# Performance work log

Measured on AMD Instinct MI355X. Metric: run time of the kernel, lower is better.

## Reference

```python
import jax, jax.numpy as jnp
import numpy as np

D_MODEL = 2048
NUM_HEADS = 16
HEAD_DIM = D_MODEL // NUM_HEADS  # 128
B, L = 2, 2048


def setup_inputs() -> dict:
    key = jax.random.key(0)
    ks = jax.random.split(key, 7)
    s = 0.02
    return {
        "x": jax.random.normal(ks[0], (B, L, D_MODEL), dtype=jnp.float32),
        "Wq_w": jax.random.normal(ks[1], (D_MODEL, D_MODEL), dtype=jnp.float32) * s,
        "Wq_b": jnp.zeros((D_MODEL,), dtype=jnp.float32),
        "Wk_w": jax.random.normal(ks[2], (HEAD_DIM, D_MODEL), dtype=jnp.float32) * s,
        "Wk_b": jnp.zeros((HEAD_DIM,), dtype=jnp.float32),
        "Wv_w": jax.random.normal(ks[3], (HEAD_DIM, D_MODEL), dtype=jnp.float32) * s,
        "Wv_b": jnp.zeros((HEAD_DIM,), dtype=jnp.float32),
    }


def reference(x, Wq_w, Wq_b, Wk_w, Wk_b, Wv_w, Wv_b):
    b, l, _ = x.shape
    # torch Linear: y = x @ W.T + b
    Q = (x @ Wq_w.T + Wq_b).reshape(b, l, NUM_HEADS, HEAD_DIM)  # [B,L,H,D]
    K = x @ Wk_w.T + Wk_b  # [B,L,D] single shared KV head (MQA)
    V = x @ Wv_w.T + Wv_b  # [B,L,D]
    scale = 1.0 / jnp.sqrt(jnp.float32(HEAD_DIM))
    # scores: [B,H,Lq,Lk]; K's head dim (size 1 in torch) broadcasts -> contract over d only
    scores = jnp.einsum("bqhd,bkd->bhqk", Q, K) * scale
    attn = jax.nn.softmax(scores, axis=-1)
    out = jnp.einsum("bhqk,bkd->bqhd", attn, V)  # [B,L,H,D]
    return out.reshape(b, l, D_MODEL)
```

## Files before the change

### kernel.cpp

```cpp
#include <hip/hip_runtime.h>
#include <hip/hip_bf16.h>


typedef unsigned short u16;
typedef unsigned int u32;
typedef __bf16 bf16x8 __attribute__((ext_vector_type(8)));
typedef float f32x16 __attribute__((ext_vector_type(16)));
typedef u16 u16x4 __attribute__((ext_vector_type(4)));
typedef u32 u32x4 __attribute__((ext_vector_type(4)));

#define MFMA32(a, b, c) __builtin_amdgcn_mfma_f32_32x32x16_bf16((a), (b), (c), 0, 0, 0)

__device__ __forceinline__ u16 f2bf(float f) {
  __hip_bfloat16 h = __float2bfloat16(f);
  return __builtin_bit_cast(u16, h);
}

__device__ __forceinline__ float fexp2(float x) {
#if __has_builtin(__builtin_amdgcn_exp2f)
  return __builtin_amdgcn_exp2f(x);
#else
  return exp2f(x);
#endif
}

__device__ __forceinline__ void cp16(const void* g, void* l) {
  __builtin_amdgcn_global_load_lds(
      (const __attribute__((address_space(1))) u32*)g,
      (__attribute__((address_space(3))) u32*)l, 16, 0, 0);
}

__device__ __forceinline__ f32x16 zero16() {
  f32x16 v;
#pragma unroll
  for (int i = 0; i < 16; ++i) v[i] = 0.f;
  return v;
}

__global__ __launch_bounds__(256) void k_convert(
    const float* __restrict__ x, const float* __restrict__ wq,
    const float* __restrict__ wk, const float* __restrict__ wv,
    u16* __restrict__ xb, u16* __restrict__ wqb,
    u16* __restrict__ wkb, u16* __restrict__ wvb) {
  int idx = blockIdx.x * 256 + threadIdx.x;
  for (int i = idx; i < 3276800; i += 524288) {
    float4 v; u16* dst;
    if (i < 2097152) {
      v = ((const float4*)x)[i]; dst = xb + (size_t)i * 4;
    } else if (i < 3145728) {
      int j = i - 2097152; v = ((const float4*)wq)[j]; dst = wqb + (size_t)j * 4;
    } else if (i < 3211264) {
      int j = i - 3145728; v = ((const float4*)wk)[j]; dst = wkb + (size_t)j * 4;
    } else {
      int j = i - 3211264; v = ((const float4*)wv)[j]; dst = wvb + (size_t)j * 4;
    }
    u16x4 o;
    o[0] = f2bf(v.x); o[1] = f2bf(v.y); o[2] = f2bf(v.z); o[3] = f2bf(v.w);
    *(u16x4*)dst = o;
  }
}

__global__ __launch_bounds__(256) void k_gemm_qkv(
    const u16* __restrict__ xb, const u16* __restrict__ wqb,
    const u16* __restrict__ wkb, const u16* __restrict__ wvb,
    const float* __restrict__ bq, const float* __restrict__ bk, const float* __restrict__ bv,
    u16* __restrict__ qout, u16* __restrict__ kout, u16* __restrict__ vtout) {
  __shared__ __align__(16) u16 sh[10240];
  const int tid = threadIdx.x;
  const int w = tid >> 6, lane = tid & 63, ln = lane & 31, hi = lane >> 5;
  const int wr = w >> 1, wc = w & 1;
  const int m0 = blockIdx.x * 128;
  const int by = blockIdx.y;
  const int mode = (by < 16) ? 0 : (by - 15);
  const int n0loc = (mode == 0) ? by * 128 : 0;
  const u16* __restrict__ Bp = (mode == 0) ? wqb : (mode == 1 ? wkb : wvb);
  const u16* Arow = xb + (size_t)m0 * 2048;
  const u16* Brow = Bp + (size_t)n0loc * 2048;

  const u16* sb[5];
#pragma unroll
  for (int i = 0; i < 5; ++i) {
    int s = (w + i * 4) * 64 + lane;
    const u16* base; int r, c;
    if (s < 640) { r = s / 5; c = s % 5; if (c > 3) c = 0; base = Arow; }
    else { int s2 = s - 640; r = s2 / 5; c = s2 % 5; if (c > 3) c = 0; base = Brow; }
    sb[i] = base + (size_t)r * 2048 + c * 8;
  }

  f32x16 acc[2][2];
  acc[0][0] = zero16(); acc[0][1] = zero16(); acc[1][0] = zero16(); acc[1][1] = zero16();

  const int a0off = (wr * 64 + ln) * 40 + hi * 8;
  const int b0off = 5120 + (wc * 64 + ln) * 40 + hi * 8;

  for (int k0 = 0; k0 < 2048; k0 += 32) {
    __syncthreads();
#pragma unroll
    for (int i = 0; i < 5; ++i)
      cp16(sb[i] + k0, (void*)(sh + (w + i * 4) * 512));
    __syncthreads();
#pragma unroll
    for (int kc = 0; kc < 2; ++kc) {
      const int ko = kc * 16;
      bf16x8 a0 = *(const bf16x8*)&sh[a0off + ko];
      bf16x8 a1 = *(const bf16x8*)&sh[a0off + 1280 + ko];
      bf16x8 b0 = *(const bf16x8*)&sh[b0off + ko];
      bf16x8 b1 = *(const bf16x8*)&sh[b0off + 1280 + ko];
      acc[0][0] = MFMA32(a0, b0, acc[0][0]);
      acc[0][1] = MFMA32(a0, b1, acc[0][1]);
      acc[1][0] = MFMA32(a1, b0, acc[1][0]);
      acc[1][1] = MFMA32(a1, b1, acc[1][1]);
    }
  }

  const float qscale = 0.12751744630098356f;
#pragma unroll
  for (int fm = 0; fm < 2; ++fm) {
#pragma unroll
    for (int fn = 0; fn < 2; ++fn) {
      f32x16 a = acc[fm][fn];
      const int mbase = m0 + wr * 64 + fm * 32;
      const int nloc = n0loc + wc * 64 + fn * 32 + ln;
      if (mode == 0) {
        const float bsc = bq[nloc] * qscale;
#pragma unroll
        for (int r = 0; r < 16; ++r) {
          int row = (r & 3) + 8 * (r >> 2) + 4 * hi;
          qout[(size_t)(mbase + row) * 2048 + nloc] = f2bf(a[r] * qscale + bsc);
        }
      } else if (mode == 1) {
        const float bb = bk[nloc];
#pragma unroll
        for (int r = 0; r < 16; ++r) {
          int row = (r & 3) + 8 * (r >> 2) + 4 * hi;
          kout[(size_t)(mbase + row) * 128 + nloc] = f2bf(a[r] + bb);
        }
      } else {
        const float bb = bv[nloc];
#pragma unroll
        for (int r = 0; r < 16; ++r) {
          int row = (r & 3) + 8 * (r >> 2) + 4 * hi;
          int m = mbase + row;
          vtout[(size_t)((m >> 11) * 128 + nloc) * 2048 + (m & 2047)] = f2bf(a[r] + bb);
        }
      }
    }
  }
}

__global__ __launch_bounds__(256, 1) void k_attn(
    const u16* __restrict__ qb, const u16* __restrict__ kb, const u16* __restrict__ vtb,
    float* __restrict__ out) {
  __shared__ __align__(16) u16 sh[35840];
  const int tid = threadIdx.x;
  const int w = tid >> 6, lane = tid & 63, ln = lane & 31, hi = lane >> 5;
  const int q0 = blockIdx.x * 256, h = blockIdx.y, b = blockIdx.z;
  const size_t bL = (size_t)b * 2048;
  const u16* kbase = kb + bL * 128;
  const u16* vbase = vtb + (size_t)b * 128 * 2048;

  bf16x8 qfA[8], qfB[8];
  {
    const u16* qrowA = qb + (bL + q0 + w * 64 + ln) * 2048 + h * 128 + hi * 8;
    const u16* qrowB = qrowA + 32 * 2048;
#pragma unroll
    for (int kc = 0; kc < 8; ++kc) {
      qfA[kc] = *(const bf16x8*)(qrowA + kc * 16);
      qfB[kc] = *(const bf16x8*)(qrowB + kc * 16);
    }
  }

  const u16* sb[9]; int smul[9];
  const int nsl = (38 - w) >> 2;
#pragma unroll
  for (int i = 0; i < 9; ++i) {
    int sl = w + i * 4;
    if (sl < 35) {
      int s = sl * 64 + lane;
      if (s < 1088) {
        int r = s / 17, c = s % 17; if (c > 15) c = 0;
        sb[i] = kbase + r * 128 + c * 8; smul[i] = 128;
      } else {
        int s2 = s - 1088; int r = s2 / 9, c = s2 % 9; if (c > 7) c = 0;
        sb[i] = vbase + (size_t)r * 2048 + c * 8; smul[i] = 1;
      }
    } else { sb[i] = kbase; smul[i] = 0; }
  }

#pragma unroll
  for (int i = 0; i < 9; ++i)
    if (i < nsl) cp16(sb[i], (void*)(sh + (w + i * 4) * 512));
  __syncthreads();

  f32x16 oA[4], oB[4];
#pragma unroll
  for (int dg = 0; dg < 4; ++dg) { oA[dg] = zero16(); oB[dg] = zero16(); }
  float lA = 0.f, lB = 0.f;

  const int kro = ln * 136 + hi * 8;
  const int vro = 8704 + ln * 72 + hi * 8;

  for (int it = 0; it < 32; ++it) {
    const int cur = (it & 1) * 17920;
    const int nxt = 17920 - cur;
    const size_t k0n = (it < 31) ? (size_t)(it + 1) * 64 : 0;
#pragma unroll
    for (int i = 0; i < 9; ++i)
      if (i < nsl) cp16(sb[i] + k0n * smul[i], (void*)(sh + nxt + (w + i * 4) * 512));

    f32x16 s0A = zero16(), s1A = zero16(), s0B = zero16(), s1B = zero16();
#pragma unroll
    for (int kc = 0; kc < 8; ++kc) {
      bf16x8 a0 = *(const bf16x8*)&sh[cur + kro + kc * 16];
      bf16x8 a1 = *(const bf16x8*)&sh[cur + kro + 32 * 136 + kc * 16];
      s0A = MFMA32(a0, qfA[kc], s0A);
      s1A = MFMA32(a1, qfA[kc], s1A);
      s0B = MFMA32(a0, qfB[kc], s0B);
      s1B = MFMA32(a1, qfB[kc], s1B);
    }

    u32 pkA[16], pkB[16];
#pragma unroll
    for (int i = 0; i < 8; ++i) {
      float a = fexp2(s0A[2 * i]), c = fexp2(s0A[2 * i + 1]);
      pkA[i] = __builtin_amdgcn_perm(__builtin_bit_cast(u32, c),
                                     __builtin_bit_cast(u32, a), 0x07060302u);
      float d = fexp2(s1A[2 * i]), e = fexp2(s1A[2 * i + 1]);
      pkA[8 + i] = __builtin_amdgcn_perm(__builtin_bit_cast(u32, e),
                                         __builtin_bit_cast(u32, d), 0x07060302u);
      float f = fexp2(s0B[2 * i]), g = fexp2(s0B[2 * i + 1]);
      pkB[i] = __builtin_amdgcn_perm(__builtin_bit_cast(u32, g),
                                     __builtin_bit_cast(u32, f), 0x07060302u);
      float p = fexp2(s1B[2 * i]), q = fexp2(s1B[2 * i + 1]);
      pkB[8 + i] = __builtin_amdgcn_perm(__builtin_bit_cast(u32, q),
                                         __builtin_bit_cast(u32, p), 0x07060302u);
    }
#pragma unroll
    for (int i = 0; i < 16; ++i) {
      lA += __builtin_bit_cast(float, pkA[i] << 16);
      lA += __builtin_bit_cast(float, pkA[i] & 0xffff0000u);
      lB += __builtin_bit_cast(float, pkB[i] << 16);
      lB += __builtin_bit_cast(float, pkB[i] & 0xffff0000u);
    }

    bf16x8 pfA[4], pfB[4];
#pragma unroll
    for (int c = 0; c < 4; ++c) {
      const int wb = 4 * c;
#pragma unroll
      for (int sel = 0; sel < 2; ++sel) {
        const u32* mat = sel ? pkB : pkA;
        u32 send0 = hi ? mat[wb] : mat[wb + 2];
        u32 send1 = hi ? mat[wb + 1] : mat[wb + 3];
        u32 r0 = (u32)__shfl_xor((int)send0, 32, 64);
        u32 r1 = (u32)__shfl_xor((int)send1, 32, 64);
        u32x4 v;
        v[0] = hi ? r0 : mat[wb];
        v[1] = hi ? r1 : mat[wb + 1];
        v[2] = hi ? mat[wb + 2] : r0;
        v[3] = hi ? mat[wb + 3] : r1;
        if (sel) pfB[c] = __builtin_bit_cast(bf16x8, v);
        else     pfA[c] = __builtin_bit_cast(bf16x8, v);
      }
    }

#pragma unroll
    for (int c = 0; c < 4; ++c)
#pragma unroll
      for (int dg = 0; dg < 4; ++dg) {
        bf16x8 va = *(const bf16x8*)&sh[cur + vro + dg * 2304 + c * 16];
        oA[dg] = MFMA32(va, pfA[c], oA[dg]);
        oB[dg] = MFMA32(va, pfB[c], oB[dg]);
      }

    __syncthreads();
  }

  lA += __shfl_xor(lA, 32, 64);
  lB += __shfl_xor(lB, 32, 64);
  const float invA = 1.0f / lA, invB = 1.0f / lB;

  float* orowA = out + (bL + q0 + w * 64 + ln) * 2048 + h * 128 + hi * 4;
  float* orowB = orowA + 32 * 2048;
#pragma unroll
  for (int dg = 0; dg < 4; ++dg)
#pragma unroll
    for (int rq = 0; rq < 4; ++rq) {
      float4 va, vb;
      va.x = oA[dg][rq * 4 + 0] * invA; va.y = oA[dg][rq * 4 + 1] * invA;
      va.z = oA[dg][rq * 4 + 2] * invA; va.w = oA[dg][rq * 4 + 3] * invA;
      vb.x = oB[dg][rq * 4 + 0] * invB; vb.y = oB[dg][rq * 4 + 1] * invB;
      vb.z = oB[dg][rq * 4 + 2] * invB; vb.w = oB[dg][rq * 4 + 3] * invB;
      *(float4*)&orowA[dg * 32 + rq * 8] = va;
      *(float4*)&orowB[dg * 32 + rq * 8] = vb;
    }
}

extern "C" void kernel_launch(void* const* d_in, const int* in_sizes, int n_in,
                              void* d_out, int out_size, void* d_ws, size_t ws_size,
                              hipStream_t stream) {
  const float* x  = (const float*)d_in[0];
  const float* wq = (const float*)d_in[1];
  const float* bq = (const float*)d_in[2];
  const float* wk = (const float*)d_in[3];
  const float* bk = (const float*)d_in[4];
  const float* wv = (const float*)d_in[5];
  const float* bv = (const float*)d_in[6];
  float* out = (float*)d_out;
  char* ws = (char*)d_ws;

  u16* xb   = (u16*)(ws);
  u16* wqb  = (u16*)(ws + 16777216);
  u16* wkb  = (u16*)(ws + 25165824);
  u16* wvb  = (u16*)(ws + 25690112);
  u16* qb   = (u16*)(ws + 26214400);
  u16* kbuf = (u16*)(ws + 42991616);
  u16* vtb  = (u16*)(ws + 44040192);

  k_convert<<<2048, 256, 0, stream>>>(x, wq, wk, wv, xb, wqb, wkb, wvb);
  k_gemm_qkv<<<dim3(32, 18), 256, 0, stream>>>(xb, wqb, wkb, wvb, bq, bk, bv, qb, kbuf, vtb);
  k_attn<<<dim3(8, 16, 2), 256, 0, stream>>>(qb, kbuf, vtb, out);
}
```

Before: 275.8 us.

## Split attention KV range across two wave groups and merge partials via LDS

The attention kernel moves to 512 threads, where two groups of four waves each process half of a 128-key tile for the same 256 queries. Loop iterations are halved and tiles doubled, and the partial outputs and row sums are reduced through shared memory at the end. The aim is more waves per CU to hide latency and more MFMA parallelism. In exchange it roughly doubles LDS use to about 136KB and adds a final reduction and barrier. Softmax has no max subtraction, so summing the unnormalized partials stays valid.

```diff
diff --git a/kernel.cpp b/kernel.cpp
--- a/kernel.cpp
+++ b/kernel.cpp
@@ -148,12 +148,13 @@
   }
 }
 
-__global__ __launch_bounds__(256, 1) void k_attn(
+__global__ __launch_bounds__(512, 2) void k_attn(
     const u16* __restrict__ qb, const u16* __restrict__ kb, const u16* __restrict__ vtb,
     float* __restrict__ out) {
-  __shared__ __align__(16) u16 sh[35840];
+  __shared__ __align__(16) u16 sh[69632];
   const int tid = threadIdx.x;
   const int w = tid >> 6, lane = tid & 63, ln = lane & 31, hi = lane >> 5;
+  const int kh = w >> 2, qblk = w & 3;
   const int q0 = blockIdx.x * 256, h = blockIdx.y, b = blockIdx.z;
   const size_t bL = (size_t)b * 2048;
   const u16* kbase = kb + bL * 128;
@@ -161,7 +162,7 @@
 
   bf16x8 qfA[8], qfB[8];
   {
-    const u16* qrowA = qb + (bL + q0 + w * 64 + ln) * 2048 + h * 128 + hi * 8;
+    const u16* qrowA = qb + (bL + q0 + qblk * 64 + ln) * 2048 + h * 128 + hi * 8;
     const u16* qrowB = qrowA + 32 * 2048;
 #pragma unroll
     for (int kc = 0; kc < 8; ++kc) {
@@ -171,25 +172,25 @@
   }
 
   const u16* sb[9]; int smul[9];
-  const int nsl = (38 - w) >> 2;
+  const int nsl = (w < 4) ? 9 : 8;
 #pragma unroll
   for (int i = 0; i < 9; ++i) {
-    int sl = w + i * 4;
-    if (sl < 35) {
+    int sl = w + i * 8;
+    if (sl < 68) {
       int s = sl * 64 + lane;
-      if (s < 1088) {
+      if (s < 2176) {
         int r = s / 17, c = s % 17; if (c > 15) c = 0;
         sb[i] = kbase + r * 128 + c * 8; smul[i] = 128;
       } else {
-        int s2 = s - 1088; int r = s2 / 9, c = s2 % 9; if (c > 7) c = 0;
-        sb[i] = vbase + (size_t)r * 2048 + c * 8; smul[i] = 1;
+        int s2 = s - 2176; int d = s2 / 17, c = s2 % 17; if (c > 15) c = 0;
+        sb[i] = vbase + (size_t)d * 2048 + c * 8; smul[i] = 1;
       }
     } else { sb[i] = kbase; smul[i] = 0; }
   }
 
 #pragma unroll
   for (int i = 0; i < 9; ++i)
-    if (i < nsl) cp16(sb[i], (void*)(sh + (w + i * 4) * 512));
+    if (i < nsl) cp16(sb[i], (void*)(sh + (w + i * 8) * 512));
   __syncthreads();
 
   f32x16 oA[4], oB[4];
@@ -197,22 +198,22 @@
   for (int dg = 0; dg < 4; ++dg) { oA[dg] = zero16(); oB[dg] = zero16(); }
   float lA = 0.f, lB = 0.f;
 
-  const int kro = ln * 136 + hi * 8;
-  const int vro = 8704 + ln * 72 + hi * 8;
-
-  for (int it = 0; it < 32; ++it) {
-    const int cur = (it & 1) * 17920;
-    const int nxt = 17920 - cur;
-    const size_t k0n = (it < 31) ? (size_t)(it + 1) * 64 : 0;
+  const int kro = (kh * 64 + ln) * 136 + hi * 8;
+  const int vro = 17408 + ln * 136 + kh * 64 + hi * 8;
+
+  for (int it = 0; it < 16; ++it) {
+    const int cur = (it & 1) * 34816;
+    const int nxt = 34816 - cur;
+    const size_t k0n = (it < 15) ? (size_t)(it + 1) * 128 : 0;
 #pragma unroll
     for (int i = 0; i < 9; ++i)
-      if (i < nsl) cp16(sb[i] + k0n * smul[i], (void*)(sh + nxt + (w + i * 4) * 512));
+      if (i < nsl) cp16(sb[i] + k0n * smul[i], (void*)(sh + nxt + (w + i * 8) * 512));
 
     f32x16 s0A = zero16(), s1A = zero16(), s0B = zero16(), s1B = zero16();
 #pragma unroll
     for (int kc = 0; kc < 8; ++kc) {
       bf16x8 a0 = *(const bf16x8*)&sh[cur + kro + kc * 16];
-      bf16x8 a1 = *(const bf16x8*)&sh[cur + kro + 32 * 136 + kc * 16];
+      bf16x8 a1 = *(const bf16x8*)&sh[cur + kro + 4352 + kc * 16];
       s0A = MFMA32(a0, qfA[kc], s0A);
       s1A = MFMA32(a1, qfA[kc], s1A);
       s0B = MFMA32(a0, qfB[kc], s0B);
@@ -268,7 +269,7 @@
     for (int c = 0; c < 4; ++c)
 #pragma unroll
       for (int dg = 0; dg < 4; ++dg) {
-        bf16x8 va = *(const bf16x8*)&sh[cur + vro + dg * 2304 + c * 16];
+        bf16x8 va = *(const bf16x8*)&sh[cur + vro + dg * 4352 + c * 16];
         oA[dg] = MFMA32(va, pfA[c], oA[dg]);
         oB[dg] = MFMA32(va, pfB[c], oB[dg]);
       }
@@ -278,22 +279,57 @@
 
   lA += __shfl_xor(lA, 32, 64);
   lB += __shfl_xor(lB, 32, 64);
-  const float invA = 1.0f / lA, invB = 1.0f / lB;
-
-  float* orowA = out + (bL + q0 + w * 64 + ln) * 2048 + h * 128 + hi * 4;
-  float* orowB = orowA + 32 * 2048;
-#pragma unroll
-  for (int dg = 0; dg < 4; ++dg)
-#pragma unroll
-    for (int rq = 0; rq < 4; ++rq) {
-      float4 va, vb;
-      va.x = oA[dg][rq * 4 + 0] * invA; va.y = oA[dg][rq * 4 + 1] * invA;
-      va.z = oA[dg][rq * 4 + 2] * invA; va.w = oA[dg][rq * 4 + 3] * invA;
-      vb.x = oB[dg][rq * 4 + 0] * invB; vb.y = oB[dg][rq * 4 + 1] * invB;
-      vb.z = oB[dg][rq * 4 + 2] * invB; vb.w = oB[dg][rq * 4 + 3] * invB;
-      *(float4*)&orowA[dg * 32 + rq * 8] = va;
-      *(float4*)&orowB[dg * 32 + rq * 8] = vb;
-    }
+
+  __syncthreads();
+  float* shf = (float*)sh;
+  float* lbuf = shf + 4 * 64 * 132;
+  if (w >= 4) {
+    float* op = shf + (w - 4) * (64 * 132);
+#pragma unroll
+    for (int dg = 0; dg < 4; ++dg)
+#pragma unroll
+      for (int rq = 0; rq < 4; ++rq) {
+        const int d = dg * 32 + rq * 8 + hi * 4;
+        float4 va, vb;
+        va.x = oA[dg][rq * 4 + 0]; va.y = oA[dg][rq * 4 + 1];
+        va.z = oA[dg][rq * 4 + 2]; va.w = oA[dg][rq * 4 + 3];
+        vb.x = oB[dg][rq * 4 + 0]; vb.y = oB[dg][rq * 4 + 1];
+        vb.z = oB[dg][rq * 4 + 2]; vb.w = oB[dg][rq * 4 + 3];
+        *(float4*)&op[ln * 132 + d] = va;
+        *(float4*)&op[(32 + ln) * 132 + d] = vb;
+      }
+    if (hi == 0) {
+      lbuf[(w - 4) * 64 + ln] = lA;
+      lbuf[(w - 4) * 64 + 32 + ln] = lB;
+    }
+  }
+  __syncthreads();
+  if (w < 4) {
+    float* op = shf + w * (64 * 132);
+    const float invA = 1.0f / (lA + lbuf[w * 64 + ln]);
+    const float invB = 1.0f / (lB + lbuf[w * 64 + 32 + ln]);
+    float* orowA = out + (bL + q0 + qblk * 64 + ln) * 2048 + h * 128 + hi * 4;
+    float* orowB = orowA + 32 * 2048;
+#pragma unroll
+    for (int dg = 0; dg < 4; ++dg)
+#pragma unroll
+      for (int rq = 0; rq < 4; ++rq) {
+        const int d = dg * 32 + rq * 8 + hi * 4;
+        float4 pa = *(const float4*)&op[ln * 132 + d];
+        float4 pb = *(const float4*)&op[(32 + ln) * 132 + d];
+        float4 va, vb;
+        va.x = (oA[dg][rq * 4 + 0] + pa.x) * invA;
+        va.y = (oA[dg][rq * 4 + 1] + pa.y) * invA;
+        va.z = (oA[dg][rq * 4 + 2] + pa.z) * invA;
+        va.w = (oA[dg][rq * 4 + 3] + pa.w) * invA;
+        vb.x = (oB[dg][rq * 4 + 0] + pb.x) * invB;
+        vb.y = (oB[dg][rq * 4 + 1] + pb.y) * invB;
+        vb.z = (oB[dg][rq * 4 + 2] + pb.z) * invB;
+        vb.w = (oB[dg][rq * 4 + 3] + pb.w) * invB;
+        *(float4*)&orowA[dg * 32 + rq * 8] = va;
+        *(float4*)&orowB[dg * 32 + rq * 8] = vb;
+      }
+  }
 }
 
 extern "C" void kernel_launch(void* const* d_in, const int* in_sizes, int n_in,
@@ -319,5 +355,5 @@
 
   k_convert<<<2048, 256, 0, stream>>>(x, wq, wk, wv, xb, wqb, wkb, wvb);
   k_gemm_qkv<<<dim3(32, 18), 256, 0, stream>>>(xb, wqb, wkb, wvb, bq, bk, bv, qb, kbuf, vtb);
-  k_attn<<<dim3(8, 16, 2), 256, 0, stream>>>(qb, kbuf, vtb, out);
-}
+  k_attn<<<dim3(8, 16, 2), 512, 0, stream>>>(qb, kbuf, vtb, out);
+}
```

Result: slower. 355.0 us (+28.7%).
